# Optimization experiments

Measured on AMD Instinct MI355X. Metric: run time of the kernel, lower is better.

The kernel has to match this reference:

```python
import jax, jax.numpy as jnp
import numpy as np

# TT config: input_dimension=2048, output_multiplier=4, rank=16
# top_ranks    = [8,2,2,2,2,2,2,2,2]  (prod = 2048)
# bottom_ranks = [8,2,2,2,2,2,2,2,2]  (prod = 2048)
# core shapes (top, bottom, left, right): left/right are TT bond ranks.
CORE_SHAPES = [(8, 8, 1, 16)] + [(2, 2, 16, 16)] * 7 + [(2, 2, 16, 1)]


def setup_inputs() -> dict:
    key = jax.random.key(0)
    ks = jax.random.split(key, 10)
    inp = {"x": jax.random.normal(ks[0], (4, 2048, 2048), dtype=jnp.float32)}
    for i, s in enumerate(CORE_SHAPES):
        inp[f"p{i}"] = jax.random.normal(ks[i + 1], s, dtype=jnp.float32)
    return inp


def _tt_apply(x, ps):
    # x: [B, S, D] with D = prod(top_ranks) = 2048
    B, S, D = x.shape
    T = B * S
    # Normalize every core to (top, bottom, left_bond_in, right_bond_out).
    # Original einsum: '... abcdefghi, ajs, bkst, cltu, dmuv, envw, fowx, gpxy, hqzy, irz -> ... jklmnopqr'
    # Core 7 ('hqzy') has swapped bonds: its 4th dim (y) is the incoming bond
    # from core 6 and its 3rd dim (z) is the outgoing bond into core 8 ('irz').
    cores = list(ps[:7]) + [jnp.transpose(ps[7], (0, 1, 3, 2)), ps[8]]
    # core 0 is used as p0[:, :, 0, :] in the original; its left dim is 1 so
    # keeping the singleton left axis is identical math.
    y = x.reshape(T, 1, 1, D)  # [T, out_so_far=1, bond=1, remaining_top=D]
    J, M = 1, D
    for g in cores:
        tk, bk, lk, rk = g.shape
        y = y.reshape(T, J, lk, tk, M // tk)
        # contract incoming bond l and current top index a with the core
        y = jnp.einsum('tjlam,ablr->tjbrm', y, g)
        J *= bk
        M //= tk
        y = y.reshape(T, J, rk, M)
    # final: rk == 1, M == 1 -> [T, J] with J = prod(bottom_ranks) = 2048
    return y.reshape(B, S, J)


def reference(x, p0, p1, p2, p3, p4, p5, p6, p7, p8):
    return _tt_apply(x, (p0, p1, p2, p3, p4, p5, p6, p7, p8))
```

## Files before the change

kernel.cpp:

```cpp
#include <hip/hip_runtime.h>
#include <stdint.h>

typedef unsigned short u16;
typedef __bf16 bf16x8 __attribute__((ext_vector_type(8)));
typedef float f32x16 __attribute__((ext_vector_type(16)));
typedef u16 u16x8 __attribute__((ext_vector_type(8)));

__device__ __forceinline__ u16 f2bf(float f) {
  uint32_t u = __float_as_uint(f);
  u += 0x7fffu + ((u >> 16) & 1u);
  return (u16)(u >> 16);
}

__global__ __launch_bounds__(256) void build_lr_kernel(
    const float* __restrict__ p0, const float* __restrict__ p1,
    const float* __restrict__ p2, const float* __restrict__ p3,
    const float* __restrict__ p4, const float* __restrict__ p5,
    const float* __restrict__ p6, const float* __restrict__ p7,
    const float* __restrict__ p8, float* __restrict__ L4, float* __restrict__ R) {
  __shared__ alignas(16) float sC[5 * 1024];
  const int tid = threadIdx.x;
  if (blockIdx.x < 64) {
    for (int i = tid; i < 1024; i += 256) {
      sC[i]        = p0[i];
      sC[1024 + i] = p1[i];
      sC[2048 + i] = p2[i];
      sC[3072 + i] = p3[i];
      sC[4096 + i] = p4[i];
    }
    __syncthreads();
    const int idx = blockIdx.x * 256 + tid;
    const int AL = idx >> 7, BL = idx & 127;
    float t[16], u[16];
    {
      const float4* c0 = (const float4*)(sC + ((AL >> 4) * 8 + (BL >> 4)) * 16);
      float4 a = c0[0], b = c0[1], c = c0[2], d = c0[3];
      t[0] = a.x; t[1] = a.y; t[2] = a.z; t[3] = a.w;
      t[4] = b.x; t[5] = b.y; t[6] = b.z; t[7] = b.w;
      t[8] = c.x; t[9] = c.y; t[10] = c.z; t[11] = c.w;
      t[12] = d.x; t[13] = d.y; t[14] = d.z; t[15] = d.w;
    }
#pragma unroll
    for (int k = 0; k < 4; k++) {
      const int ak = (AL >> (3 - k)) & 1;
      const int bk = (BL >> (3 - k)) & 1;
      const float* ck = sC + (k + 1) * 1024 + ((ak * 2 + bk) << 8);
#pragma unroll
      for (int r = 0; r < 16; r++) u[r] = 0.f;
#pragma unroll
      for (int l = 0; l < 16; l++) {
        const float4 ca = *(const float4*)(ck + l * 16);
        const float4 cb = *(const float4*)(ck + l * 16 + 4);
        const float4 cc = *(const float4*)(ck + l * 16 + 8);
        const float4 cd = *(const float4*)(ck + l * 16 + 12);
        const float tv = t[l];
        u[0] += tv * ca.x;  u[1] += tv * ca.y;  u[2] += tv * ca.z;  u[3] += tv * ca.w;
        u[4] += tv * cb.x;  u[5] += tv * cb.y;  u[6] += tv * cb.z;  u[7] += tv * cb.w;
        u[8] += tv * cc.x;  u[9] += tv * cc.y;  u[10] += tv * cc.z; u[11] += tv * cc.w;
        u[12] += tv * cd.x; u[13] += tv * cd.y; u[14] += tv * cd.z; u[15] += tv * cd.w;
      }
#pragma unroll
      for (int r = 0; r < 16; r++) t[r] = u[r];
    }
    float4* dst = (float4*)(L4 + (size_t)idx * 16);
#pragma unroll
    for (int j = 0; j < 4; j++)
      dst[j] = make_float4(t[4 * j], t[4 * j + 1], t[4 * j + 2], t[4 * j + 3]);
  } else {
    for (int i = tid; i < 1024; i += 256) {
      sC[i]        = p5[i];
      sC[1024 + i] = p6[i];
      sC[2048 + i] = p7[i];
    }
    for (int i = tid; i < 64; i += 256) sC[3072 + i] = p8[i];
    __syncthreads();
    const int AR = tid >> 4, BR = tid & 15;
    const int a5 = AR >> 3, a6 = (AR >> 2) & 1, a7 = (AR >> 1) & 1, a8 = AR & 1;
    const int b5 = BR >> 3, b6 = (BR >> 2) & 1, b7 = (BR >> 1) & 1, b8 = BR & 1;
    float t[16], u[16];
    {
      const float4* c8 = (const float4*)(sC + 3072 + (a8 * 2 + b8) * 16);
      float4 a = c8[0], b = c8[1], c = c8[2], d = c8[3];
      t[0] = a.x; t[1] = a.y; t[2] = a.z; t[3] = a.w;
      t[4] = b.x; t[5] = b.y; t[6] = b.z; t[7] = b.w;
      t[8] = c.x; t[9] = c.y; t[10] = c.z; t[11] = c.w;
      t[12] = d.x; t[13] = d.y; t[14] = d.z; t[15] = d.w;
    }
    {
      const float* c7 = sC + 2048 + ((a7 * 2 + b7) << 8);
#pragma unroll
      for (int r = 0; r < 16; r++) u[r] = 0.f;
#pragma unroll
      for (int z = 0; z < 16; z++) {
        const float4 ca = *(const float4*)(c7 + z * 16);
        const float4 cb = *(const float4*)(c7 + z * 16 + 4);
        const float4 cc = *(const float4*)(c7 + z * 16 + 8);
        const float4 cd = *(const float4*)(c7 + z * 16 + 12);
        const float tv = t[z];
        u[0] += tv * ca.x;  u[1] += tv * ca.y;  u[2] += tv * ca.z;  u[3] += tv * ca.w;
        u[4] += tv * cb.x;  u[5] += tv * cb.y;  u[6] += tv * cb.z;  u[7] += tv * cb.w;
        u[8] += tv * cc.x;  u[9] += tv * cc.y;  u[10] += tv * cc.z; u[11] += tv * cc.w;
        u[12] += tv * cd.x; u[13] += tv * cd.y; u[14] += tv * cd.z; u[15] += tv * cd.w;
      }
#pragma unroll
      for (int r = 0; r < 16; r++) t[r] = u[r];
    }
    {
      const float* c6 = sC + 1024 + ((a6 * 2 + b6) << 8);
#pragma unroll
      for (int rl = 0; rl < 16; rl++) {
        const float4 ca = *(const float4*)(c6 + rl * 16);
        const float4 cb = *(const float4*)(c6 + rl * 16 + 4);
        const float4 cc = *(const float4*)(c6 + rl * 16 + 8);
        const float4 cd = *(const float4*)(c6 + rl * 16 + 12);
        float s = 0.f;
        s += t[0] * ca.x;  s += t[1] * ca.y;  s += t[2] * ca.z;  s += t[3] * ca.w;
        s += t[4] * cb.x;  s += t[5] * cb.y;  s += t[6] * cb.z;  s += t[7] * cb.w;
        s += t[8] * cc.x;  s += t[9] * cc.y;  s += t[10] * cc.z; s += t[11] * cc.w;
        s += t[12] * cd.x; s += t[13] * cd.y; s += t[14] * cd.z; s += t[15] * cd.w;
        u[rl] = s;
      }
#pragma unroll
      for (int r = 0; r < 16; r++) t[r] = u[r];
    }
    {
      const float* c5 = sC + ((a5 * 2 + b5) << 8);
#pragma unroll
      for (int rl = 0; rl < 16; rl++) {
        const float4 ca = *(const float4*)(c5 + rl * 16);
        const float4 cb = *(const float4*)(c5 + rl * 16 + 4);
        const float4 cc = *(const float4*)(c5 + rl * 16 + 8);
        const float4 cd = *(const float4*)(c5 + rl * 16 + 12);
        float s = 0.f;
        s += t[0] * ca.x;  s += t[1] * ca.y;  s += t[2] * ca.z;  s += t[3] * ca.w;
        s += t[4] * cb.x;  s += t[5] * cb.y;  s += t[6] * cb.z;  s += t[7] * cb.w;
        s += t[8] * cc.x;  s += t[9] * cc.y;  s += t[10] * cc.z; s += t[11] * cc.w;
        s += t[12] * cd.x; s += t[13] * cd.y; s += t[14] * cd.z; s += t[15] * cd.w;
        R[tid * 16 + rl] = s;
      }
    }
  }
}

__global__ __launch_bounds__(256) void prep_kernel(const float* __restrict__ L4,
                                                   const float* __restrict__ R,
                                                   u16* __restrict__ Wt,
                                                   const float* __restrict__ x,
                                                   u16* __restrict__ xb) {
  if (blockIdx.x < 2048) {
    int t = blockIdx.x * 256 + threadIdx.x;
    int e = t * 8;
    int Af = e & 2047;
    int Bf = e >> 11;
    const float* lrow = L4 + ((Af >> 4) * 128 + (Bf >> 4)) * 16;
    float lv[16];
#pragma unroll
    for (int r = 0; r < 16; r++) lv[r] = lrow[r];
    const float* rbase = R + (Bf & 15) * 16;
    u16x8 o;
#pragma unroll
    for (int j = 0; j < 8; j++) {
      const float* rrow = rbase + ((Af + j) & 15) * 256;
      float s = 0.f;
#pragma unroll
      for (int r = 0; r < 16; r++) s += lv[r] * rrow[r];
      o[j] = f2bf(s);
    }
    *(u16x8*)(Wt + (size_t)Bf * 2048 + Af) = o;
  } else {
    size_t i = ((size_t)(blockIdx.x - 2048) * 256 + threadIdx.x) * 8;
    float4 u = *(const float4*)(x + i);
    float4 v = *(const float4*)(x + i + 4);
    u16x8 o;
    o[0] = f2bf(u.x); o[1] = f2bf(u.y); o[2] = f2bf(u.z); o[3] = f2bf(u.w);
    o[4] = f2bf(v.x); o[5] = f2bf(v.y); o[6] = f2bf(v.z); o[7] = f2bf(v.w);
    *(u16x8*)(xb + i) = o;
  }
}

#define SB0() __builtin_amdgcn_sched_barrier(0)
#define LGKM(n) asm volatile("s_waitcnt lgkmcnt(" #n ")" ::: "memory")
#define VMCW(n) asm volatile("s_waitcnt vmcnt(" #n ")" ::: "memory")
#define BAR() asm volatile("s_barrier" ::: "memory")

#define STAGE1(Sbase, dsto, gp, uoff)                                          \
  __builtin_amdgcn_global_load_lds(                                            \
      (const __attribute__((address_space(1))) void*)((gp) + (uoff) + pl),     \
      (__attribute__((address_space(3))) void*)((Sbase) + (dsto) + ldst), 16, 0, 0)

#define STAGE_A(h, dsto, gk)                                                   \
  STAGE1(As, (dsto), A, uA + ((h)*128) * 2048 + (gk));                         \
  STAGE1(As, (dsto) + 4096, A, uA + ((h)*128 + 64) * 2048 + (gk))

#define STAGE_B(h, dsto, gk)                                                   \
  STAGE1(Bs, (dsto), B, uB + ((h)*128) * 2048 + (gk));                         \
  STAGE1(Bs, (dsto) + 4096, B, uB + ((h)*128 + 64) * 2048 + (gk))

#define READ_KS(aS, bS, ks, base)                                              \
  _Pragma("unroll") for (int ah_ = 0; ah_ < 2; ah_++)                          \
      _Pragma("unroll") for (int m_ = 0; m_ < 2; m_++)                         \
          aS[ah_][m_] = *(const bf16x8*)(As + (base) + ah_ * 8192 + rbA +      \
                                         m_ * 2048 + ((((ks)*2 + hl) ^ key) * 8)); \
  _Pragma("unroll") for (int bh_ = 0; bh_ < 2; bh_++)                          \
      bS[bh_] = *(const bf16x8*)(Bs + (base) + bh_ * 8192 + rbB +              \
                                 ((((ks)*2 + hl) ^ key) * 8))

#define MFMA_KS(aS, bS)                                                        \
  acc[0][0][0] = __builtin_amdgcn_mfma_f32_32x32x16_bf16(aS[0][0], bS[0], acc[0][0][0], 0, 0, 0); \
  acc[1][0][0] = __builtin_amdgcn_mfma_f32_32x32x16_bf16(aS[1][0], bS[0], acc[1][0][0], 0, 0, 0); \
  acc[0][1][0] = __builtin_amdgcn_mfma_f32_32x32x16_bf16(aS[0][0], bS[1], acc[0][1][0], 0, 0, 0); \
  acc[1][1][0] = __builtin_amdgcn_mfma_f32_32x32x16_bf16(aS[1][0], bS[1], acc[1][1][0], 0, 0, 0); \
  acc[0][0][1] = __builtin_amdgcn_mfma_f32_32x32x16_bf16(aS[0][1], bS[0], acc[0][0][1], 0, 0, 0); \
  acc[1][0][1] = __builtin_amdgcn_mfma_f32_32x32x16_bf16(aS[1][1], bS[0], acc[1][0][1], 0, 0, 0); \
  acc[0][1][1] = __builtin_amdgcn_mfma_f32_32x32x16_bf16(aS[0][1], bS[1], acc[0][1][1], 0, 0, 0); \
  acc[1][1][1] = __builtin_amdgcn_mfma_f32_32x32x16_bf16(aS[1][1], bS[1], acc[1][1][1], 0, 0, 0)

__global__ __launch_bounds__(512, 2) void gemm_kernel(const u16* __restrict__ A,
                                                      const u16* __restrict__ B,
                                                      float* __restrict__ C) {
  __shared__ alignas(128) u16 As[4 * 8192];
  __shared__ alignas(128) u16 Bs[4 * 8192];
  const int tid = threadIdx.x;
  const int lane = tid & 63;
  const int w = tid >> 6;
  const int wr = w >> 2;
  const int wc = w & 3;
  const int r32 = lane & 31;
  const int hl = lane >> 5;

  const int F = blockIdx.x + (blockIdx.y << 3);
  const int li = F >> 3;
  const int m0 = ((F & 7) * 4 + (li >> 3)) << 8;
  const int n0 = (li & 7) << 8;

  const int srow = lane >> 3;
  const int soct = (lane & 7) ^ srow;
  const int uA = m0 * 2048;
  const int uB = n0 * 2048;
  const int pl = (w * 8 + srow) * 2048 + soct * 8;
  const int ldst = w * 512;

  const int key = r32 & 7;
  const int rbA = (wr * 64 + r32) * 64;
  const int rbB = (wc * 32 + r32) * 64;

  f32x16 acc[2][2][2] = {};
  bf16x8 a0_[2][2], b0_[2];
  bf16x8 a1_[2][2], b1_[2];

  STAGE_A(0, 0, 0); STAGE_A(1, 8192, 0);
  STAGE_B(0, 0, 0); STAGE_B(1, 8192, 0);
  VMCW(0);
  BAR();
  SB0();
  READ_KS(a0_, b0_, 0, 0);
  SB0();

#pragma unroll 1
  for (int t = 0; t < 32; t++) {
    const int pav = (t & 1) << 14;
    const int pnv = 16384 - pav;
    const int k1 = (t < 31 ? t + 1 : 31) * 64;
    STAGE_A(0, pnv, k1); STAGE_A(1, pnv + 8192, k1);
    STAGE_B(0, pnv, k1); STAGE_B(1, pnv + 8192, k1);
    SB0();
    READ_KS(a1_, b1_, 1, pav);
    SB0();
    LGKM(6); SB0();
    __builtin_amdgcn_s_setprio(1);
    MFMA_KS(a0_, b0_);
    __builtin_amdgcn_s_setprio(0);
    SB0();
    READ_KS(a0_, b0_, 2, pav);
    SB0();
    LGKM(6); SB0();
    __builtin_amdgcn_s_setprio(1);
    MFMA_KS(a1_, b1_);
    __builtin_amdgcn_s_setprio(0);
    SB0();
    READ_KS(a1_, b1_, 3, pav);
    SB0();
    LGKM(6); SB0();
    __builtin_amdgcn_s_setprio(1);
    MFMA_KS(a0_, b0_);
    __builtin_amdgcn_s_setprio(0);
    SB0();
    VMCW(0);
    BAR();
    SB0();
    READ_KS(a0_, b0_, 0, pnv);
    SB0();
    LGKM(6); SB0();
    __builtin_amdgcn_s_setprio(1);
    MFMA_KS(a1_, b1_);
    __builtin_amdgcn_s_setprio(0);
    SB0();
    BAR();
    SB0();
  }

  LGKM(0);
  VMCW(0);

#pragma unroll
  for (int ah = 0; ah < 2; ah++)
#pragma unroll
    for (int bh = 0; bh < 2; bh++)
#pragma unroll
      for (int m = 0; m < 2; m++) {
        size_t cbase = (size_t)(m0 + ah * 128 + wr * 64 + m * 32 + 4 * hl) * 2048 +
                       (n0 + bh * 128 + wc * 32 + r32);
#pragma unroll
        for (int reg = 0; reg < 16; reg++) {
          int row = (reg & 3) + 8 * (reg >> 2);
          __builtin_nontemporal_store(acc[ah][bh][m][reg], C + cbase + (size_t)row * 2048);
        }
      }
}

extern "C" void kernel_launch(void* const* d_in, const int* in_sizes, int n_in,
                              void* d_out, int out_size, void* d_ws, size_t ws_size,
                              hipStream_t stream) {
  const float* x = (const float*)d_in[0];
  const float* p0 = (const float*)d_in[1];
  const float* p1 = (const float*)d_in[2];
  const float* p2 = (const float*)d_in[3];
  const float* p3 = (const float*)d_in[4];
  const float* p4 = (const float*)d_in[5];
  const float* p5 = (const float*)d_in[6];
  const float* p6 = (const float*)d_in[7];
  const float* p7 = (const float*)d_in[8];
  const float* p8 = (const float*)d_in[9];
  char* ws = (char*)d_ws;
  u16* xbf = (u16*)ws;
  u16* Wt = (u16*)(ws + 33554432);
  float* L4 = (float*)(ws + 41943040);
  float* R = (float*)(ws + 42991616);

  build_lr_kernel<<<65, 256, 0, stream>>>(p0, p1, p2, p3, p4, p5, p6, p7, p8, L4, R);
  prep_kernel<<<10240, 256, 0, stream>>>(L4, R, Wt, x, xbf);
  gemm_kernel<<<dim3(8, 32), 512, 0, stream>>>(xbf, Wt, (float*)d_out);
}
```

Measured before the change: 221.9 us.

## Fuse TT left/right partial-product construction into the weight-materialization kernel

Removes the separate build_lr kernel launch and its global L4/R intermediates. Each Wt row block now loads the core slices it needs into shared memory, computes its 128 left partial products and 16 right partial products on chip, and expands them into the bf16 weight row. This drops one launch and a global round trip for the intermediates. In exchange, the left/right products are recomputed redundantly across 2048 blocks, and only 144 of 256 threads do work in that phase.

```diff
diff --git a/kernel.cpp b/kernel.cpp
--- a/kernel.cpp
+++ b/kernel.cpp
@@ -12,161 +12,156 @@
   return (u16)(u >> 16);
 }
 
-__global__ __launch_bounds__(256) void build_lr_kernel(
+__global__ __launch_bounds__(256) void prep_kernel(
     const float* __restrict__ p0, const float* __restrict__ p1,
     const float* __restrict__ p2, const float* __restrict__ p3,
     const float* __restrict__ p4, const float* __restrict__ p5,
     const float* __restrict__ p6, const float* __restrict__ p7,
-    const float* __restrict__ p8, float* __restrict__ L4, float* __restrict__ R) {
-  __shared__ alignas(16) float sC[5 * 1024];
+    const float* __restrict__ p8, u16* __restrict__ Wt,
+    const float* __restrict__ x, u16* __restrict__ xb) {
+  __shared__ alignas(16) float S[6624];
   const int tid = threadIdx.x;
-  if (blockIdx.x < 64) {
-    for (int i = tid; i < 1024; i += 256) {
-      sC[i]        = p0[i];
-      sC[1024 + i] = p1[i];
-      sC[2048 + i] = p2[i];
-      sC[3072 + i] = p3[i];
-      sC[4096 + i] = p4[i];
+  if (blockIdx.x < 2048) {
+    const int bx = blockIdx.x;
+    const int BL = bx >> 4, BR = bx & 15;
+    const int B0 = BL >> 4;
+    const int b1 = (BL >> 3) & 1, b2 = (BL >> 2) & 1, b3 = (BL >> 1) & 1, b4 = BL & 1;
+    const int b5 = (BR >> 3) & 1, b6 = (BR >> 2) & 1, b7 = (BR >> 1) & 1, b8 = BR & 1;
+    if (tid < 128) S[tid] = p0[((tid >> 4) * 8 + B0) * 16 + (tid & 15)];
+    for (int i = tid; i < 512; i += 256) S[128 + i]  = p1[(((i >> 8) * 2 + b1) << 8) + (i & 255)];
+    for (int i = tid; i < 512; i += 256) S[640 + i]  = p2[(((i >> 8) * 2 + b2) << 8) + (i & 255)];
+    for (int i = tid; i < 512; i += 256) S[1152 + i] = p3[(((i >> 8) * 2 + b3) << 8) + (i & 255)];
+    for (int i = tid; i < 512; i += 256) S[1664 + i] = p4[(((i >> 8) * 2 + b4) << 8) + (i & 255)];
+    for (int i = tid; i < 512; i += 256) S[2176 + i] = p5[(((i >> 8) * 2 + b5) << 8) + (i & 255)];
+    for (int i = tid; i < 512; i += 256) S[2688 + i] = p6[(((i >> 8) * 2 + b6) << 8) + (i & 255)];
+    for (int i = tid; i < 512; i += 256) S[3200 + i] = p7[(((i >> 8) * 2 + b7) << 8) + (i & 255)];
+    if (tid < 32) S[3712 + tid] = p8[((tid >> 4) * 2 + b8) * 16 + (tid & 15)];
+    __syncthreads();
+    if (tid < 128) {
+      const int AL = tid;
+      float t[16], u[16];
+      {
+        const float4* c0 = (const float4*)(S + (AL >> 4) * 16);
+        float4 a = c0[0], b = c0[1], c = c0[2], d = c0[3];
+        t[0] = a.x; t[1] = a.y; t[2] = a.z; t[3] = a.w;
+        t[4] = b.x; t[5] = b.y; t[6] = b.z; t[7] = b.w;
+        t[8] = c.x; t[9] = c.y; t[10] = c.z; t[11] = c.w;
+        t[12] = d.x; t[13] = d.y; t[14] = d.z; t[15] = d.w;
+      }
+#pragma unroll
+      for (int k = 0; k < 4; k++) {
+        const int ak = (AL >> (3 - k)) & 1;
+        const float* ck = S + 128 + k * 512 + (ak << 8);
+#pragma unroll
+        for (int r = 0; r < 16; r++) u[r] = 0.f;
+#pragma unroll
+        for (int l = 0; l < 16; l++) {
+          const float4 ca = *(const float4*)(ck + l * 16);
+          const float4 cb = *(const float4*)(ck + l * 16 + 4);
+          const float4 cc = *(const float4*)(ck + l * 16 + 8);
+          const float4 cd = *(const float4*)(ck + l * 16 + 12);
+          const float tv = t[l];
+          u[0] += tv * ca.x;  u[1] += tv * ca.y;  u[2] += tv * ca.z;  u[3] += tv * ca.w;
+          u[4] += tv * cb.x;  u[5] += tv * cb.y;  u[6] += tv * cb.z;  u[7] += tv * cb.w;
+          u[8] += tv * cc.x;  u[9] += tv * cc.y;  u[10] += tv * cc.z; u[11] += tv * cc.w;
+          u[12] += tv * cd.x; u[13] += tv * cd.y; u[14] += tv * cd.z; u[15] += tv * cd.w;
+        }
+#pragma unroll
+        for (int r = 0; r < 16; r++) t[r] = u[r];
+      }
+      float* dl = S + 3744 + AL * 20;
+      *(float4*)(dl)      = make_float4(t[0], t[1], t[2], t[3]);
+      *(float4*)(dl + 4)  = make_float4(t[4], t[5], t[6], t[7]);
+      *(float4*)(dl + 8)  = make_float4(t[8], t[9], t[10], t[11]);
+      *(float4*)(dl + 12) = make_float4(t[12], t[13], t[14], t[15]);
+    } else if (tid < 144) {
+      const int AR = tid & 15;
+      const int a5 = (AR >> 3) & 1, a6 = (AR >> 2) & 1, a7 = (AR >> 1) & 1, a8 = AR & 1;
+      float t[16], u[16];
+      {
+        const float4* c8 = (const float4*)(S + 3712 + a8 * 16);
+        float4 a = c8[0], b = c8[1], c = c8[2], d = c8[3];
+        t[0] = a.x; t[1] = a.y; t[2] = a.z; t[3] = a.w;
+        t[4] = b.x; t[5] = b.y; t[6] = b.z; t[7] = b.w;
+        t[8] = c.x; t[9] = c.y; t[10] = c.z; t[11] = c.w;
+        t[12] = d.x; t[13] = d.y; t[14] = d.z; t[15] = d.w;
+      }
+      {
+        const float* c7 = S + 3200 + (a7 << 8);
+#pragma unroll
+        for (int r = 0; r < 16; r++) u[r] = 0.f;
+#pragma unroll
+        for (int z = 0; z < 16; z++) {
+          const float4 ca = *(const float4*)(c7 + z * 16);
+          const float4 cb = *(const float4*)(c7 + z * 16 + 4);
+          const float4 cc = *(const float4*)(c7 + z * 16 + 8);
+          const float4 cd = *(const float4*)(c7 + z * 16 + 12);
+          const float tv = t[z];
+          u[0] += tv * ca.x;  u[1] += tv * ca.y;  u[2] += tv * ca.z;  u[3] += tv * ca.w;
+          u[4] += tv * cb.x;  u[5] += tv * cb.y;  u[6] += tv * cb.z;  u[7] += tv * cb.w;
+          u[8] += tv * cc.x;  u[9] += tv * cc.y;  u[10] += tv * cc.z; u[11] += tv * cc.w;
+          u[12] += tv * cd.x; u[13] += tv * cd.y; u[14] += tv * cd.z; u[15] += tv * cd.w;
+        }
+#pragma unroll
+        for (int r = 0; r < 16; r++) t[r] = u[r];
+      }
+      {
+        const float* c6 = S + 2688 + (a6 << 8);
+#pragma unroll
+        for (int rl = 0; rl < 16; rl++) {
+          const float4 ca = *(const float4*)(c6 + rl * 16);
+          const float4 cb = *(const float4*)(c6 + rl * 16 + 4);
+          const float4 cc = *(const float4*)(c6 + rl * 16 + 8);
+          const float4 cd = *(const float4*)(c6 + rl * 16 + 12);
+          float s = 0.f;
+          s += t[0] * ca.x;  s += t[1] * ca.y;  s += t[2] * ca.z;  s += t[3] * ca.w;
+          s += t[4] * cb.x;  s += t[5] * cb.y;  s += t[6] * cb.z;  s += t[7] * cb.w;
+          s += t[8] * cc.x;  s += t[9] * cc.y;  s += t[10] * cc.z; s += t[11] * cc.w;
+          s += t[12] * cd.x; s += t[13] * cd.y; s += t[14] * cd.z; s += t[15] * cd.w;
+          u[rl] = s;
+        }
+#pragma unroll
+        for (int r = 0; r < 16; r++) t[r] = u[r];
+      }
+      {
+        const float* c5 = S + 2176 + (a5 << 8);
+#pragma unroll
+        for (int rl = 0; rl < 16; rl++) {
+          const float4 ca = *(const float4*)(c5 + rl * 16);
+          const float4 cb = *(const float4*)(c5 + rl * 16 + 4);
+          const float4 cc = *(const float4*)(c5 + rl * 16 + 8);
+          const float4 cd = *(const float4*)(c5 + rl * 16 + 12);
+          float s = 0.f;
+          s += t[0] * ca.x;  s += t[1] * ca.y;  s += t[2] * ca.z;  s += t[3] * ca.w;
+          s += t[4] * cb.x;  s += t[5] * cb.y;  s += t[6] * cb.z;  s += t[7] * cb.w;
+          s += t[8] * cc.x;  s += t[9] * cc.y;  s += t[10] * cc.z; s += t[11] * cc.w;
+          s += t[12] * cd.x; s += t[13] * cd.y; s += t[14] * cd.z; s += t[15] * cd.w;
+          S[6304 + AR * 20 + rl] = s;
+        }
+      }
     }
     __syncthreads();
-    const int idx = blockIdx.x * 256 + tid;
-    const int AL = idx >> 7, BL = idx & 127;
-    float t[16], u[16];
+    const int KH = tid >> 1;
+    const float* lp = S + 3744 + KH * 20;
+    float lv[16];
     {
-      const float4* c0 = (const float4*)(sC + ((AL >> 4) * 8 + (BL >> 4)) * 16);
-      float4 a = c0[0], b = c0[1], c = c0[2], d = c0[3];
-      t[0] = a.x; t[1] = a.y; t[2] = a.z; t[3] = a.w;
-      t[4] = b.x; t[5] = b.y; t[6] = b.z; t[7] = b.w;
-      t[8] = c.x; t[9] = c.y; t[10] = c.z; t[11] = c.w;
-      t[12] = d.x; t[13] = d.y; t[14] = d.z; t[15] = d.w;
+      float4 a = *(const float4*)(lp), b = *(const float4*)(lp + 4);
+      float4 c = *(const float4*)(lp + 8), d = *(const float4*)(lp + 12);
+      lv[0] = a.x; lv[1] = a.y; lv[2] = a.z; lv[3] = a.w;
+      lv[4] = b.x; lv[5] = b.y; lv[6] = b.z; lv[7] = b.w;
+      lv[8] = c.x; lv[9] = c.y; lv[10] = c.z; lv[11] = c.w;
+      lv[12] = d.x; lv[13] = d.y; lv[14] = d.z; lv[15] = d.w;
     }
-#pragma unroll
-    for (int k = 0; k < 4; k++) {
-      const int ak = (AL >> (3 - k)) & 1;
-      const int bk = (BL >> (3 - k)) & 1;
-      const float* ck = sC + (k + 1) * 1024 + ((ak * 2 + bk) << 8);
-#pragma unroll
-      for (int r = 0; r < 16; r++) u[r] = 0.f;
-#pragma unroll
-      for (int l = 0; l < 16; l++) {
-        const float4 ca = *(const float4*)(ck + l * 16);
-        const float4 cb = *(const float4*)(ck + l * 16 + 4);
-        const float4 cc = *(const float4*)(ck + l * 16 + 8);
-        const float4 cd = *(const float4*)(ck + l * 16 + 12);
-        const float tv = t[l];
-        u[0] += tv * ca.x;  u[1] += tv * ca.y;  u[2] += tv * ca.z;  u[3] += tv * ca.w;
-        u[4] += tv * cb.x;  u[5] += tv * cb.y;  u[6] += tv * cb.z;  u[7] += tv * cb.w;
-        u[8] += tv * cc.x;  u[9] += tv * cc.y;  u[10] += tv * cc.z; u[11] += tv * cc.w;
-        u[12] += tv * cd.x; u[13] += tv * cd.y; u[14] += tv * cd.z; u[15] += tv * cd.w;
-      }
-#pragma unroll
-      for (int r = 0; r < 16; r++) t[r] = u[r];
-    }
-    float4* dst = (float4*)(L4 + (size_t)idx * 16);
-#pragma unroll
-    for (int j = 0; j < 4; j++)
-      dst[j] = make_float4(t[4 * j], t[4 * j + 1], t[4 * j + 2], t[4 * j + 3]);
-  } else {
-    for (int i = tid; i < 1024; i += 256) {
-      sC[i]        = p5[i];
-      sC[1024 + i] = p6[i];
-      sC[2048 + i] = p7[i];
-    }
-    for (int i = tid; i < 64; i += 256) sC[3072 + i] = p8[i];
-    __syncthreads();
-    const int AR = tid >> 4, BR = tid & 15;
-    const int a5 = AR >> 3, a6 = (AR >> 2) & 1, a7 = (AR >> 1) & 1, a8 = AR & 1;
-    const int b5 = BR >> 3, b6 = (BR >> 2) & 1, b7 = (BR >> 1) & 1, b8 = BR & 1;
-    float t[16], u[16];
-    {
-      const float4* c8 = (const float4*)(sC + 3072 + (a8 * 2 + b8) * 16);
-      float4 a = c8[0], b = c8[1], c = c8[2], d = c8[3];
-      t[0] = a.x; t[1] = a.y; t[2] = a.z; t[3] = a.w;
-      t[4] = b.x; t[5] = b.y; t[6] = b.z; t[7] = b.w;
-      t[8] = c.x; t[9] = c.y; t[10] = c.z; t[11] = c.w;
-      t[12] = d.x; t[13] = d.y; t[14] = d.z; t[15] = d.w;
-    }
-    {
-      const float* c7 = sC + 2048 + ((a7 * 2 + b7) << 8);
-#pragma unroll
-      for (int r = 0; r < 16; r++) u[r] = 0.f;
-#pragma unroll
-      for (int z = 0; z < 16; z++) {
-        const float4 ca = *(const float4*)(c7 + z * 16);
-        const float4 cb = *(const float4*)(c7 + z * 16 + 4);
-        const float4 cc = *(const float4*)(c7 + z * 16 + 8);
-        const float4 cd = *(const float4*)(c7 + z * 16 + 12);
-        const float tv = t[z];
-        u[0] += tv * ca.x;  u[1] += tv * ca.y;  u[2] += tv * ca.z;  u[3] += tv * ca.w;
-        u[4] += tv * cb.x;  u[5] += tv * cb.y;  u[6] += tv * cb.z;  u[7] += tv * cb.w;
-        u[8] += tv * cc.x;  u[9] += tv * cc.y;  u[10] += tv * cc.z; u[11] += tv * cc.w;
-        u[12] += tv * cd.x; u[13] += tv * cd.y; u[14] += tv * cd.z; u[15] += tv * cd.w;
-      }
-#pragma unroll
-      for (int r = 0; r < 16; r++) t[r] = u[r];
-    }
-    {
-      const float* c6 = sC + 1024 + ((a6 * 2 + b6) << 8);
-#pragma unroll
-      for (int rl = 0; rl < 16; rl++) {
-        const float4 ca = *(const float4*)(c6 + rl * 16);
-        const float4 cb = *(const float4*)(c6 + rl * 16 + 4);
-        const float4 cc = *(const float4*)(c6 + rl * 16 + 8);
-        const float4 cd = *(const float4*)(c6 + rl * 16 + 12);
-        float s = 0.f;
-        s += t[0] * ca.x;  s += t[1] * ca.y;  s += t[2] * ca.z;  s += t[3] * ca.w;
-        s += t[4] * cb.x;  s += t[5] * cb.y;  s += t[6] * cb.z;  s += t[7] * cb.w;
-        s += t[8] * cc.x;  s += t[9] * cc.y;  s += t[10] * cc.z; s += t[11] * cc.w;
-        s += t[12] * cd.x; s += t[13] * cd.y; s += t[14] * cd.z; s += t[15] * cd.w;
-        u[rl] = s;
-      }
-#pragma unroll
-      for (int r = 0; r < 16; r++) t[r] = u[r];
-    }
-    {
-      const float* c5 = sC + ((a5 * 2 + b5) << 8);
-#pragma unroll
-      for (int rl = 0; rl < 16; rl++) {
-        const float4 ca = *(const float4*)(c5 + rl * 16);
-        const float4 cb = *(const float4*)(c5 + rl * 16 + 4);
-        const float4 cc = *(const float4*)(c5 + rl * 16 + 8);
-        const float4 cd = *(const float4*)(c5 + rl * 16 + 12);
-        float s = 0.f;
-        s += t[0] * ca.x;  s += t[1] * ca.y;  s += t[2] * ca.z;  s += t[3] * ca.w;
-        s += t[4] * cb.x;  s += t[5] * cb.y;  s += t[6] * cb.z;  s += t[7] * cb.w;
-        s += t[8] * cc.x;  s += t[9] * cc.y;  s += t[10] * cc.z; s += t[11] * cc.w;
-        s += t[12] * cd.x; s += t[13] * cd.y; s += t[14] * cd.z; s += t[15] * cd.w;
-        R[tid * 16 + rl] = s;
-      }
-    }
-  }
-}
-
-__global__ __launch_bounds__(256) void prep_kernel(const float* __restrict__ L4,
-                                                   const float* __restrict__ R,
-                                                   u16* __restrict__ Wt,
-                                                   const float* __restrict__ x,
-                                                   u16* __restrict__ xb) {
-  if (blockIdx.x < 2048) {
-    int t = blockIdx.x * 256 + threadIdx.x;
-    int e = t * 8;
-    int Af = e & 2047;
-    int Bf = e >> 11;
-    const float* lrow = L4 + ((Af >> 4) * 128 + (Bf >> 4)) * 16;
-    float lv[16];
-#pragma unroll
-    for (int r = 0; r < 16; r++) lv[r] = lrow[r];
-    const float* rbase = R + (Bf & 15) * 16;
     u16x8 o;
 #pragma unroll
     for (int j = 0; j < 8; j++) {
-      const float* rrow = rbase + ((Af + j) & 15) * 256;
+      const float* rr = S + 6304 + ((tid & 1) * 8 + j) * 20;
       float s = 0.f;
 #pragma unroll
-      for (int r = 0; r < 16; r++) s += lv[r] * rrow[r];
+      for (int r = 0; r < 16; r++) s += lv[r] * rr[r];
       o[j] = f2bf(s);
     }
-    *(u16x8*)(Wt + (size_t)Bf * 2048 + Af) = o;
+    *(u16x8*)(Wt + (size_t)bx * 2048 + tid * 8) = o;
   } else {
     size_t i = ((size_t)(blockIdx.x - 2048) * 256 + threadIdx.x) * 8;
     float4 u = *(const float4*)(x + i);
@@ -334,10 +329,8 @@
   char* ws = (char*)d_ws;
   u16* xbf = (u16*)ws;
   u16* Wt = (u16*)(ws + 33554432);
-  float* L4 = (float*)(ws + 41943040);
-  float* R = (float*)(ws + 42991616);
-
-  build_lr_kernel<<<65, 256, 0, stream>>>(p0, p1, p2, p3, p4, p5, p6, p7, p8, L4, R);
-  prep_kernel<<<10240, 256, 0, stream>>>(L4, R, Wt, x, xbf);
+
+  prep_kernel<<<10240, 256, 0, stream>>>(p0, p1, p2, p3, p4, p5, p6, p7, p8,
+                                         Wt, x, xbf);
   gemm_kernel<<<dim3(8, 32), 512, 0, stream>>>(xbf, Wt, (float*)d_out);
 }
```

Result: slower. 231.8 us (+4.5%).

## Use 4 waves per GEMM block with 128x128 per-wave output tiles

Applied to the files above, without the earlier changes.

The GEMM block drops from 8 waves (512 threads) to 4 waves (256 threads). Each wave now computes a 128x128 sub-tile using a 4x4 grid of 32x32 MFMA accumulators instead of 2x2x2. Each wave issues more global-to-LDS loads and LDS fragment reads per k-step. The LDS-fragment-to-MFMA ratio rises, cutting LDS read traffic per FLOP. In exchange it roughly doubles accumulator register use (256 AGPR/VGPR for acc) and lowers the number of waves available to hide latency.

```diff
diff --git a/kernel.cpp b/kernel.cpp
--- a/kernel.cpp
+++ b/kernel.cpp
@@ -183,39 +183,35 @@
 #define VMCW(n) asm volatile("s_waitcnt vmcnt(" #n ")" ::: "memory")
 #define BAR() asm volatile("s_barrier" ::: "memory")
 
-#define STAGE1(Sbase, dsto, gp, uoff)                                          \
+#define GLDS(gaddr, laddr)                                                     \
   __builtin_amdgcn_global_load_lds(                                            \
-      (const __attribute__((address_space(1))) void*)((gp) + (uoff) + pl),     \
-      (__attribute__((address_space(3))) void*)((Sbase) + (dsto) + ldst), 16, 0, 0)
-
-#define STAGE_A(h, dsto, gk)                                                   \
-  STAGE1(As, (dsto), A, uA + ((h)*128) * 2048 + (gk));                         \
-  STAGE1(As, (dsto) + 4096, A, uA + ((h)*128 + 64) * 2048 + (gk))
-
-#define STAGE_B(h, dsto, gk)                                                   \
-  STAGE1(Bs, (dsto), B, uB + ((h)*128) * 2048 + (gk));                         \
-  STAGE1(Bs, (dsto) + 4096, B, uB + ((h)*128 + 64) * 2048 + (gk))
+      (const __attribute__((address_space(1))) void*)(gaddr),                  \
+      (__attribute__((address_space(3))) void*)(laddr), 16, 0, 0)
+
+#define STAGE_TILE(dstp, gk)                                                   \
+  _Pragma("unroll") for (int h_ = 0; h_ < 2; h_++)                             \
+      _Pragma("unroll") for (int q_ = 0; q_ < 4; q_++) {                       \
+    GLDS(A + uA + (size_t)(h_ * 128 + w * 32 + q_ * 8) * 2048 + (gk) + pl,     \
+         As + (dstp) + h_ * 8192 + w * 2048 + q_ * 512);                       \
+    GLDS(B + uB + (size_t)(h_ * 128 + w * 32 + q_ * 8) * 2048 + (gk) + pl,     \
+         Bs + (dstp) + h_ * 8192 + w * 2048 + q_ * 512);                       \
+  }
 
 #define READ_KS(aS, bS, ks, base)                                              \
-  _Pragma("unroll") for (int ah_ = 0; ah_ < 2; ah_++)                          \
-      _Pragma("unroll") for (int m_ = 0; m_ < 2; m_++)                         \
-          aS[ah_][m_] = *(const bf16x8*)(As + (base) + ah_ * 8192 + rbA +      \
-                                         m_ * 2048 + ((((ks)*2 + hl) ^ key) * 8)); \
-  _Pragma("unroll") for (int bh_ = 0; bh_ < 2; bh_++)                          \
-      bS[bh_] = *(const bf16x8*)(Bs + (base) + bh_ * 8192 + rbB +              \
-                                 ((((ks)*2 + hl) ^ key) * 8))
+  _Pragma("unroll") for (int m_ = 0; m_ < 4; m_++)                             \
+      aS[m_] = *(const bf16x8*)(As + (base) + wr * 8192 +                      \
+                                (m_ * 32 + r32) * 64 + ((((ks)*2 + hl) ^ key) * 8)); \
+  _Pragma("unroll") for (int n_ = 0; n_ < 4; n_++)                             \
+      bS[n_] = *(const bf16x8*)(Bs + (base) + wc * 8192 +                      \
+                                (n_ * 32 + r32) * 64 + ((((ks)*2 + hl) ^ key) * 8))
 
 #define MFMA_KS(aS, bS)                                                        \
-  acc[0][0][0] = __builtin_amdgcn_mfma_f32_32x32x16_bf16(aS[0][0], bS[0], acc[0][0][0], 0, 0, 0); \
-  acc[1][0][0] = __builtin_amdgcn_mfma_f32_32x32x16_bf16(aS[1][0], bS[0], acc[1][0][0], 0, 0, 0); \
-  acc[0][1][0] = __builtin_amdgcn_mfma_f32_32x32x16_bf16(aS[0][0], bS[1], acc[0][1][0], 0, 0, 0); \
-  acc[1][1][0] = __builtin_amdgcn_mfma_f32_32x32x16_bf16(aS[1][0], bS[1], acc[1][1][0], 0, 0, 0); \
-  acc[0][0][1] = __builtin_amdgcn_mfma_f32_32x32x16_bf16(aS[0][1], bS[0], acc[0][0][1], 0, 0, 0); \
-  acc[1][0][1] = __builtin_amdgcn_mfma_f32_32x32x16_bf16(aS[1][1], bS[0], acc[1][0][1], 0, 0, 0); \
-  acc[0][1][1] = __builtin_amdgcn_mfma_f32_32x32x16_bf16(aS[0][1], bS[1], acc[0][1][1], 0, 0, 0); \
-  acc[1][1][1] = __builtin_amdgcn_mfma_f32_32x32x16_bf16(aS[1][1], bS[1], acc[1][1][1], 0, 0, 0)
-
-__global__ __launch_bounds__(512, 2) void gemm_kernel(const u16* __restrict__ A,
+  _Pragma("unroll") for (int m_ = 0; m_ < 4; m_++)                             \
+      _Pragma("unroll") for (int n_ = 0; n_ < 4; n_++)                         \
+          acc[m_][n_] = __builtin_amdgcn_mfma_f32_32x32x16_bf16(               \
+              aS[m_], bS[n_], acc[m_][n_], 0, 0, 0)
+
+__global__ __launch_bounds__(256, 1) void gemm_kernel(const u16* __restrict__ A,
                                                       const u16* __restrict__ B,
                                                       float* __restrict__ C) {
   __shared__ alignas(128) u16 As[4 * 8192];
@@ -223,8 +219,8 @@
   const int tid = threadIdx.x;
   const int lane = tid & 63;
   const int w = tid >> 6;
-  const int wr = w >> 2;
-  const int wc = w & 3;
+  const int wr = w >> 1;
+  const int wc = w & 1;
   const int r32 = lane & 31;
   const int hl = lane >> 5;
 
@@ -237,23 +233,19 @@
   const int soct = (lane & 7) ^ srow;
   const int uA = m0 * 2048;
   const int uB = n0 * 2048;
-  const int pl = (w * 8 + srow) * 2048 + soct * 8;
-  const int ldst = w * 512;
+  const int pl = srow * 2048 + soct * 8;
 
   const int key = r32 & 7;
-  const int rbA = (wr * 64 + r32) * 64;
-  const int rbB = (wc * 32 + r32) * 64;
-
-  f32x16 acc[2][2][2] = {};
-  bf16x8 a0_[2][2], b0_[2];
-  bf16x8 a1_[2][2], b1_[2];
-
-  STAGE_A(0, 0, 0); STAGE_A(1, 8192, 0);
-  STAGE_B(0, 0, 0); STAGE_B(1, 8192, 0);
+
+  f32x16 acc[4][4] = {};
+  bf16x8 aA[4], bA[4];
+  bf16x8 aB[4], bB[4];
+
+  STAGE_TILE(0, 0);
   VMCW(0);
   BAR();
   SB0();
-  READ_KS(a0_, b0_, 0, 0);
+  READ_KS(aA, bA, 0, 0);
   SB0();
 
 #pragma unroll 1
@@ -261,38 +253,37 @@
     const int pav = (t & 1) << 14;
     const int pnv = 16384 - pav;
     const int k1 = (t < 31 ? t + 1 : 31) * 64;
-    STAGE_A(0, pnv, k1); STAGE_A(1, pnv + 8192, k1);
-    STAGE_B(0, pnv, k1); STAGE_B(1, pnv + 8192, k1);
-    SB0();
-    READ_KS(a1_, b1_, 1, pav);
-    SB0();
-    LGKM(6); SB0();
+    STAGE_TILE(pnv, k1);
+    SB0();
+    READ_KS(aB, bB, 1, pav);
+    SB0();
+    LGKM(8); SB0();
     __builtin_amdgcn_s_setprio(1);
-    MFMA_KS(a0_, b0_);
+    MFMA_KS(aA, bA);
     __builtin_amdgcn_s_setprio(0);
     SB0();
-    READ_KS(a0_, b0_, 2, pav);
-    SB0();
-    LGKM(6); SB0();
+    READ_KS(aA, bA, 2, pav);
+    SB0();
+    LGKM(8); SB0();
     __builtin_amdgcn_s_setprio(1);
-    MFMA_KS(a1_, b1_);
+    MFMA_KS(aB, bB);
     __builtin_amdgcn_s_setprio(0);
     SB0();
-    READ_KS(a1_, b1_, 3, pav);
-    SB0();
-    LGKM(6); SB0();
+    READ_KS(aB, bB, 3, pav);
+    SB0();
+    LGKM(8); SB0();
     __builtin_amdgcn_s_setprio(1);
-    MFMA_KS(a0_, b0_);
+    MFMA_KS(aA, bA);
     __builtin_amdgcn_s_setprio(0);
     SB0();
     VMCW(0);
     BAR();
     SB0();
-    READ_KS(a0_, b0_, 0, pnv);
-    SB0();
-    LGKM(6); SB0();
+    READ_KS(aA, bA, 0, pnv);
+    SB0();
+    LGKM(8); SB0();
     __builtin_amdgcn_s_setprio(1);
-    MFMA_KS(a1_, b1_);
+    MFMA_KS(aB, bB);
     __builtin_amdgcn_s_setprio(0);
     SB0();
     BAR();
@@ -303,19 +294,17 @@
   VMCW(0);
 
 #pragma unroll
-  for (int ah = 0; ah < 2; ah++)
-#pragma unroll
-    for (int bh = 0; bh < 2; bh++)
-#pragma unroll
-      for (int m = 0; m < 2; m++) {
-        size_t cbase = (size_t)(m0 + ah * 128 + wr * 64 + m * 32 + 4 * hl) * 2048 +
-                       (n0 + bh * 128 + wc * 32 + r32);
-#pragma unroll
-        for (int reg = 0; reg < 16; reg++) {
-          int row = (reg & 3) + 8 * (reg >> 2);
-          __builtin_nontemporal_store(acc[ah][bh][m][reg], C + cbase + (size_t)row * 2048);
-        }
-      }
+  for (int m_ = 0; m_ < 4; m_++)
+#pragma unroll
+    for (int n_ = 0; n_ < 4; n_++) {
+      size_t cbase = (size_t)(m0 + wr * 128 + m_ * 32 + 4 * hl) * 2048 +
+                     (n0 + wc * 128 + n_ * 32 + r32);
+#pragma unroll
+      for (int reg = 0; reg < 16; reg++) {
+        int row = (reg & 3) + 8 * (reg >> 2);
+        __builtin_nontemporal_store(acc[m_][n_][reg], C + cbase + (size_t)row * 2048);
+      }
+    }
 }
 
 extern "C" void kernel_launch(void* const* d_in, const int* in_sizes, int n_in,
@@ -339,5 +328,5 @@
 
   build_lr_kernel<<<65, 256, 0, stream>>>(p0, p1, p2, p3, p4, p5, p6, p7, p8, L4, R);
   prep_kernel<<<10240, 256, 0, stream>>>(L4, R, Wt, x, xbf);
-  gemm_kernel<<<dim3(8, 32), 512, 0, stream>>>(xbf, Wt, (float*)d_out);
-}
+  gemm_kernel<<<dim3(8, 32), 256, 0, stream>>>(xbf, Wt, (float*)d_out);
+}
```

After: 227.4 us. 1.02x slower.
